# Kernel tuning notes

Measured on AMD Instinct MI355X. Metric: run time of the kernel, lower is better.

The kernel has to match this reference:

```python
import jax, jax.numpy as jnp
import numpy as np

N = 50000       # nodes
E = 1600000     # directed edges (avg degree 32)
H = 2           # heads (layers 1-2)
F_IN = 128
F_HID = 64      # per-head hidden channels
F_OUT = 64
SCALE = 0.05


def setup_inputs() -> dict:
    key = jax.random.key(0)
    ks = jax.random.split(key, 15)

    def p(k, shape):
        return jax.random.normal(k, shape, jnp.float32) * SCALE

    x = jax.random.normal(ks[0], (N, F_IN), jnp.float32)
    edge_index = jax.random.randint(ks[1], (2, E), 0, N, dtype=jnp.int64)
    return dict(
        x=x,
        W1=p(ks[2], (F_IN, H * F_HID)), as1=p(ks[3], (H, F_HID)), ad1=p(ks[4], (H, F_HID)), b1=p(ks[5], (H * F_HID,)),
        W2=p(ks[6], (H * F_HID, H * F_HID)), as2=p(ks[7], (H, F_HID)), ad2=p(ks[8], (H, F_HID)), b2=p(ks[9], (H * F_HID,)),
        W3=p(ks[10], (H * F_HID, F_OUT)), as3=p(ks[11], (1, F_OUT)), ad3=p(ks[12], (1, F_OUT)), b3=p(ks[13], (F_OUT,)),
        edge_index=edge_index,
    )


def gat_layer(x, W, a_src, a_dst, b, src, dst, heads, f_out):
    """One PyG-style GATConv (concat=True, negative_slope=0.2), dropout off (eval)."""
    n = x.shape[0]
    h = (x @ W).reshape(n, heads, f_out)                 # [N,H,F]
    al_s = jnp.einsum('nhf,hf->nh', h, a_src)            # (x_j * att_src).sum(-1)
    al_d = jnp.einsum('nhf,hf->nh', h, a_dst)
    e = jax.nn.leaky_relu(al_s[src] + al_d[dst], 0.2)    # [Etot,H]
    # segment softmax over incoming edges of each dst node
    m = jax.lax.stop_gradient(jax.ops.segment_max(e, dst, num_segments=n))
    ee = jnp.exp(e - m[dst])
    denom = jax.ops.segment_sum(ee, dst, num_segments=n)
    alpha = ee / (denom[dst] + 1e-16)                    # [Etot,H]
    out = jax.ops.segment_sum(h[src] * alpha[:, :, None], dst, num_segments=n)
    return out.reshape(n, heads * f_out) + b


def reference(x, W1, as1, ad1, b1, W2, as2, ad2, b2, W3, as3, ad3, b3, edge_index):
    # add_self_loops=True (PyG default): same augmented edge set for all layers
    loops = jnp.arange(N, dtype=edge_index.dtype)
    src = jnp.concatenate([edge_index[0], loops])
    dst = jnp.concatenate([edge_index[1], loops])
    h = jax.nn.elu(gat_layer(x, W1, as1, ad1, b1, src, dst, H, F_HID))
    h = jax.nn.elu(gat_layer(h, W2, as2, ad2, b2, src, dst, H, F_HID))
    h = jax.nn.elu(gat_layer(h, W3, as3, ad3, b3, src, dst, 1, F_OUT))
    return h
```

## Files before the change

kernel.cpp:

```cpp
#include <hip/hip_runtime.h>
#include <hip/hip_bf16.h>
#include <hip/hip_fp16.h>


#define ELU(x) ((x) > 0.f ? (x) : (__expf(x) - 1.f))
#define BSH 8
#define CHK 8192

typedef _Float16 f16x8 __attribute__((ext_vector_type(8)));
typedef float    f32x4 __attribute__((ext_vector_type(4)));
typedef float    f32x2 __attribute__((ext_vector_type(2)));

__device__ inline unsigned int f16x4_to_fp8(__half2 h0, __half2 h1) {
    float2 a = __half22float2(h0), b = __half22float2(h1);
    unsigned int r = __builtin_amdgcn_cvt_pk_fp8_f32(a.x, a.y, 0, false);
    r = __builtin_amdgcn_cvt_pk_fp8_f32(b.x, b.y, r, true);
    return r;
}

__global__ __launch_bounds__(1024) void phase0(
    const float* __restrict__ W1, __half* __restrict__ Wt1,
    const float* __restrict__ W2, __half* __restrict__ Wt2,
    const float* __restrict__ W3, __half* __restrict__ Wt3,
    const int* __restrict__ ei, int* __restrict__ bhist_rows, int E_)
{
    const int t = threadIdx.x;
    const int b = blockIdx.x;
    if (b < 40) {
        int idx = b * 1024 + t;
        const float* W; __half* Wt; int N;
        if (idx < 16384)      { W = W1; Wt = Wt1; N = 128; }
        else if (idx < 32768) { W = W2; Wt = Wt2; N = 128; idx -= 16384; }
        else                  { W = W3; Wt = Wt3; N = 64;  idx -= 32768; }
        int nn = idx >> 7, k = idx & 127;
        Wt[idx] = __float2half(W[k * N + nn]);
    } else {
        __shared__ int cnt[256];
        int hb = b - 40;
        if (t < 256) cnt[t] = 0;
        __syncthreads();
        const int e0 = hb * CHK;
        for (int i = t; i < CHK; i += 1024) {
            int e = e0 + i;
            if (e >= E_) break;
            atomicAdd(&cnt[ei[E_ + e] >> BSH], 1);
        }
        __syncthreads();
        if (t < 256) bhist_rows[hb * 256 + t] = cnt[t];
    }
}

__global__ __launch_bounds__(1024) void scan_bases(
    const int* __restrict__ bhist_rows, int* __restrict__ boff,
    int* __restrict__ bases, int* __restrict__ part, int HB, int n, int NB)
{
    __shared__ int part4[4][256];
    __shared__ int tot[256];
    __shared__ int col[256];
    const int t = threadIdx.x;
    const int b = blockIdx.x;

    {
        const int tcol = t & 255, grp = t >> 8;
        int v = 0;
        for (int r = grp; r < HB; r += 4) v += bhist_rows[r * 256 + tcol];
        part4[grp][tcol] = v;
    }
    __syncthreads();
    if (t < 256) {
        int v = part4[0][t] + part4[1][t] + part4[2][t] + part4[3][t];
        int nodes_t = n - (t << BSH);
        nodes_t = nodes_t < 0 ? 0 : (nodes_t > 256 ? 256 : nodes_t);
        tot[t] = (t < NB) ? (v + nodes_t) : 0;
    }
    __syncthreads();
    for (int d = 1; d < 256; d <<= 1) {
        int x = 0;
        if (t < 256 && t >= d) x = tot[t - d];
        __syncthreads();
        if (t < 256 && t >= d) tot[t] += x;
        __syncthreads();
    }
    if (b == 0) {
        if (t < NB) boff[t + 1] = tot[t];
        if (t == 0) boff[0] = 0;
    }
    const int base0 = (b > 0) ? tot[b - 1] : 0;
    const int bend  = tot[b];

    if (t < 256) col[t] = (t < HB) ? bhist_rows[t * 256 + b] : 0;
    __syncthreads();
    for (int d = 1; d < 256; d <<= 1) {
        int x = 0;
        if (t < 256 && t >= d) x = col[t - d];
        __syncthreads();
        if (t < 256 && t >= d) col[t] += x;
        __syncthreads();
    }
    if (t < HB) {
        int c = bhist_rows[t * 256 + b];
        bases[b * HB + t] = base0 + col[t] - c;
    }

    const int n0 = b << BSH;
    const int nodes = min(256, n - n0);
    const int sl0 = bend - nodes;
    if (t < nodes) part[sl0 + t] = (n0 + t) | (t << 16);
}

__global__ __launch_bounds__(1024) void edge_partition(
    const int* __restrict__ ei, const int* __restrict__ bases,
    int* __restrict__ part, int E_, int HB, int NB)
{
    __shared__ int cnt[256];
    __shared__ int sbase[256];
    const int t = threadIdx.x;
    const int hb = blockIdx.x;
    if (t < 256) {
        cnt[t] = 0;
        sbase[t] = (t < NB) ? bases[t * HB + hb] : 0;
    }
    __syncthreads();
    const int e0 = hb * CHK;
    for (int i = t; i < CHK; i += 1024) {
        int e = e0 + i;
        if (e >= E_) break;
        int src = ei[e], dst = ei[E_ + e];
        int b = dst >> BSH;
        int pos = sbase[b] + atomicAdd(&cnt[b], 1);
        part[pos] = src | ((dst & 255) << 16);
    }
}

__global__ __launch_bounds__(1024) void bucket_fill(
    const int* __restrict__ boff, const int* __restrict__ part,
    unsigned short* __restrict__ csr, int* __restrict__ off, int n)
{
    __shared__ int sm[256];
    __shared__ int cur[256];
    __shared__ int slice[12544];
    const int t = threadIdx.x;
    const int b = blockIdx.x;
    const int n0 = b << BSH;
    const int nodes = min(256, n - n0);
    const int off0 = boff[b];
    const int sz = boff[b + 1] - off0;

    if (t < 256) cur[t] = 0;
    __syncthreads();
    for (int i = t; i < sz; i += 1024)
        atomicAdd(&cur[(part[off0 + i] >> 16) & 255], 1);
    __syncthreads();
    int v = 0;
    if (t < 256) { v = cur[t]; sm[t] = v; }
    __syncthreads();
    for (int d = 1; d < 256; d <<= 1) {
        int x = 0;
        if (t < 256 && t >= d) x = sm[t - d];
        __syncthreads();
        if (t < 256 && t >= d) sm[t] += x;
        __syncthreads();
    }
    if (t < 256) {
        const int excl = sm[t] - v;
        if (t < nodes) off[n0 + t] = off0 + excl;
        if (t == nodes - 1) off[n0 + nodes] = off0 + sz;
        cur[t] = excl;
    }
    __syncthreads();

    if (sz <= 12544) {
        for (int i = t; i < sz; i += 1024) {
            int p  = part[off0 + i];
            int dl = (p >> 16) & 255;
            int pos = atomicAdd(&cur[dl], 1);
            slice[pos] = p & 0xFFFF;
        }
        __syncthreads();
        for (int i = t; i < sz; i += 1024)
            csr[off0 + i] = (unsigned short)slice[i];
    } else {
        for (int i = t; i < sz; i += 1024) {
            int p  = part[off0 + i];
            int dl = (p >> 16) & 255;
            int pos = atomicAdd(&cur[dl], 1);
            csr[off0 + pos] = (unsigned short)(p & 0xFFFF);
        }
    }
}

__global__ __launch_bounds__(256) void gemm1_mfma(
    const float* __restrict__ A, const __half* __restrict__ Wt,
    unsigned char* __restrict__ Hout, const float* __restrict__ a_s,
    const float* __restrict__ a_d, float* __restrict__ alS,
    float* __restrict__ alD, int nrows)
{
    constexpr int N = 128, NT = 8, WR = 136;
    __shared__ _Float16 wt[N * WR];
    __shared__ _Float16 hst[4][16 * WR];

    const int t = threadIdx.x, w = t >> 6, l = t & 63;
    const int q = l >> 4, n = l & 15;
    const int node0 = blockIdx.x * 64;
    const int row_base = node0 + w * 16;

    for (int i = t; i < N * 16; i += 256) {
        int r = i >> 4, c = i & 15;
        float4 v = *(const float4*)&Wt[r * 128 + c * 8];
        *(float4*)&wt[r * WR + c * 8] = v;
    }
    __syncthreads();

    f32x4 acc[NT];
#pragma unroll
    for (int ct = 0; ct < NT; ct++) acc[ct] = (f32x4){0.f, 0.f, 0.f, 0.f};

    int arow = row_base + n; if (arow >= nrows) arow = nrows - 1;
    const float* Ap = A + (size_t)arow * 128 + q * 8;
#pragma unroll
    for (int ks = 0; ks < 4; ks++) {
        float4 va = *(const float4*)(Ap + ks * 32);
        float4 vb = *(const float4*)(Ap + ks * 32 + 4);
        f16x8 a = { (_Float16)va.x, (_Float16)va.y, (_Float16)va.z, (_Float16)va.w,
                    (_Float16)vb.x, (_Float16)vb.y, (_Float16)vb.z, (_Float16)vb.w };
#pragma unroll
        for (int ct = 0; ct < NT; ct++) {
            f16x8 bb = *(const f16x8*)&wt[(ct * 16 + n) * WR + ks * 32 + q * 8];
            acc[ct] = __builtin_amdgcn_mfma_f32_16x16x32_f16(a, bb, acc[ct], 0, 0, 0);
        }
    }

    float asv[NT], adv[NT];
#pragma unroll
    for (int ct = 0; ct < NT; ct++) {
        asv[ct] = a_s[ct * 16 + n];
        adv[ct] = a_d[ct * 16 + n];
    }
#pragma unroll
    for (int r = 0; r < 4; r++) {
        int grow = row_base + q * 4 + r;
        float s0 = 0.f, d0 = 0.f, s1 = 0.f, d1 = 0.f;
#pragma unroll
        for (int ct = 0; ct < NT; ct++) {
            float v = acc[ct][r];
            float ps = v * asv[ct], pd = v * adv[ct];
            if (ct >= 4) { s1 += ps; d1 += pd; }
            else         { s0 += ps; d0 += pd; }
        }
#pragma unroll
        for (int m = 1; m < 16; m <<= 1) {
            s0 += __shfl_xor(s0, m); d0 += __shfl_xor(d0, m);
            s1 += __shfl_xor(s1, m); d1 += __shfl_xor(d1, m);
        }
        if (n == 0 && grow < nrows) {
            alS[grow * 2] = s0;     alD[grow * 2] = d0;
            alS[grow * 2 + 1] = s1; alD[grow * 2 + 1] = d1;
        }
    }

#pragma unroll
    for (int ct = 0; ct < NT; ct++)
#pragma unroll
        for (int r = 0; r < 4; r++)
            hst[w][(q * 4 + r) * WR + ct * 16 + n] = (_Float16)acc[ct][r];
    __syncthreads();
    {
        int row = l >> 2, c = l & 3;
        int grow = row_base + row;
        if (grow < nrows) {
#pragma unroll
            for (int i = 0; i < 4; i++) {
                float4 v = *(float4*)&hst[w][row * WR + c * 32 + i * 8];
                const __half2* hp = (const __half2*)&v;
                uint2 o;
                o.x = f16x4_to_fp8(hp[0], hp[1]);
                o.y = f16x4_to_fp8(hp[2], hp[3]);
                *(uint2*)&Hout[(size_t)grow * 128 + c * 32 + i * 8] = o;
            }
        }
    }
}

template<int OUTN>
__global__ __launch_bounds__(256) void gat_gather_gemm(
    const int* __restrict__ off, const unsigned short* __restrict__ csr,
    const unsigned char* __restrict__ h, const float* __restrict__ alS,
    const float* __restrict__ alD, const float* __restrict__ bias,
    const __half* __restrict__ Wt, const float* __restrict__ a_s,
    const float* __restrict__ a_d, unsigned char* __restrict__ Hout,
    float* __restrict__ alSo, float* __restrict__ alDo, int n)
{
    constexpr int HF = 128, WR = 136;
    constexpr int CTW = OUTN / 64;
    constexpr int CPW = OUTN / 4;
    constexpr int C = 768;
    __shared__ _Float16 actT[16 * WR];
    __shared__ float red_s[4][16], red_d[4][16];
    __shared__ int soff[17];
    __shared__ unsigned short esrc[C];
    __shared__ float ew[2][C];

    const int t = threadIdx.x;
    const int node0 = blockIdx.x * 16;

    if (t < 17) {
        int nd = node0 + t; nd = nd < n ? nd : n;
        soff[t] = off[nd];
    }
    __syncthreads();
    const int blk0 = soff[0];
    const int blkE = soff[16] - blk0;

    const int l = t & 15;
    const int nl = t >> 4;
    const int c0 = l * 8;
    const int head = l >> 3;
    const int s0 = soff[nl] - blk0;
    const int s1 = soff[nl + 1] - blk0;

    float a0 = 0.f, a1 = 0.f, a2 = 0.f, a3 = 0.f;
    float a4 = 0.f, a5 = 0.f, a6 = 0.f, a7 = 0.f, wsum = 0.f;

    for (int cbase = 0; cbase < blkE; cbase += C) {
        const int cend = min(blkE, cbase + C);

        for (int i = cbase + t; i < cend; i += 256) {
            int src = csr[blk0 + i];
            int lo = 0, hi = 16;
            while (hi - lo > 1) {
                int mid = (lo + hi) >> 1;
                if (soff[mid] - blk0 <= i) lo = mid; else hi = mid;
            }
            int dst = node0 + lo;
            float2 as2 = *(const float2*)&alS[src * 2];
            float2 ad2 = *(const float2*)&alD[dst * 2];
            float e0 = as2.x + ad2.x; e0 = e0 > 0.f ? e0 : 0.2f * e0;
            float e1 = as2.y + ad2.y; e1 = e1 > 0.f ? e1 : 0.2f * e1;
            esrc[i - cbase] = (unsigned short)src;
            ew[0][i - cbase] = __expf(e0);
            ew[1][i - cbase] = __expf(e1);
        }
        __syncthreads();

        const int lo = (s0 > cbase ? s0 : cbase) - cbase;
        const int hi = (s1 < cend ? s1 : cend) - cbase;
        if (lo < hi) {
            int sk[4]; float wk[4]; uint2 hv[4];
#pragma unroll
            for (int k = 0; k < 4; k++) {
                int jj = lo + k < hi ? lo + k : hi - 1;
                sk[k] = esrc[jj];
                wk[k] = (lo + k < hi) ? ew[head][jj] : 0.f;
            }
#pragma unroll
            for (int k = 0; k < 4; k++)
                hv[k] = *(const uint2*)&h[(size_t)sk[k] * HF + c0];

            for (int j = lo; j < hi; j += 4) {
                int ns[4]; float nw[4]; uint2 nv[4];
#pragma unroll
                for (int k = 0; k < 4; k++) {
                    int jj = j + 4 + k < hi ? j + 4 + k : hi - 1;
                    ns[k] = esrc[jj];
                    nw[k] = (j + 4 + k < hi) ? ew[head][jj] : 0.f;
                }
#pragma unroll
                for (int k = 0; k < 4; k++)
                    nv[k] = *(const uint2*)&h[(size_t)ns[k] * HF + c0];
#pragma unroll
                for (int k = 0; k < 4; k++) {
                    float w = wk[k];
                    f32x2 f0 = __builtin_amdgcn_cvt_pk_f32_fp8(hv[k].x, false);
                    f32x2 f1 = __builtin_amdgcn_cvt_pk_f32_fp8(hv[k].x, true);
                    f32x2 f2 = __builtin_amdgcn_cvt_pk_f32_fp8(hv[k].y, false);
                    f32x2 f3 = __builtin_amdgcn_cvt_pk_f32_fp8(hv[k].y, true);
                    a0 = fmaf(w, f0.x, a0); a1 = fmaf(w, f0.y, a1);
                    a2 = fmaf(w, f1.x, a2); a3 = fmaf(w, f1.y, a3);
                    a4 = fmaf(w, f2.x, a4); a5 = fmaf(w, f2.y, a5);
                    a6 = fmaf(w, f3.x, a6); a7 = fmaf(w, f3.y, a7);
                    wsum += w;
                }
#pragma unroll
                for (int k = 0; k < 4; k++) { sk[k] = ns[k]; wk[k] = nw[k]; hv[k] = nv[k]; }
            }
        }
        __syncthreads();
    }

    {
        const float inv = 1.f / (wsum + 1e-16f);
        float4 b0 = *(const float4*)&bias[c0];
        float4 b1 = *(const float4*)&bias[c0 + 4];
        float o[8];
        o[0] = ELU(fmaf(a0, inv, b0.x));
        o[1] = ELU(fmaf(a1, inv, b0.y));
        o[2] = ELU(fmaf(a2, inv, b0.z));
        o[3] = ELU(fmaf(a3, inv, b0.w));
        o[4] = ELU(fmaf(a4, inv, b1.x));
        o[5] = ELU(fmaf(a5, inv, b1.y));
        o[6] = ELU(fmaf(a6, inv, b1.z));
        o[7] = ELU(fmaf(a7, inv, b1.w));
        __half2 p[4];
#pragma unroll
        for (int k = 0; k < 4; k++) p[k] = __floats2half2_rn(o[2 * k], o[2 * k + 1]);
        *(float4*)&actT[nl * WR + l * 8] = *(float4*)p;
    }
    __syncthreads();

    const int w = t >> 6, l64 = t & 63, q = l64 >> 4, nn = l64 & 15;
    const __half* Wp = Wt + (size_t)(w * CPW + nn) * 128 + q * 8;
    f32x4 acc[CTW];
#pragma unroll
    for (int ct = 0; ct < CTW; ct++) acc[ct] = (f32x4){0.f, 0.f, 0.f, 0.f};
#pragma unroll
    for (int ks = 0; ks < 4; ks++) {
        f16x8 a = *(const f16x8*)&actT[nn * WR + ks * 32 + q * 8];
#pragma unroll
        for (int ct = 0; ct < CTW; ct++) {
            f16x8 bb = *(const f16x8*)(Wp + ct * 16 * 128 + ks * 32);
            acc[ct] = __builtin_amdgcn_mfma_f32_16x16x32_f16(a, bb, acc[ct], 0, 0, 0);
        }
    }

    float asv[CTW], adv2[CTW];
#pragma unroll
    for (int ct = 0; ct < CTW; ct++) {
        asv[ct]  = a_s[w * CPW + ct * 16 + nn];
        adv2[ct] = a_d[w * CPW + ct * 16 + nn];
    }
#pragma unroll
    for (int r = 0; r < 4; r++) {
        float s = 0.f, d = 0.f;
#pragma unroll
        for (int ct = 0; ct < CTW; ct++) {
            float vv = acc[ct][r];
            s = fmaf(vv, asv[ct], s);
            d = fmaf(vv, adv2[ct], d);
        }
#pragma unroll
        for (int m = 1; m < 16; m <<= 1) {
            s += __shfl_xor(s, m);
            d += __shfl_xor(d, m);
        }
        if (nn == 0) { red_s[w][q * 4 + r] = s; red_d[w][q * 4 + r] = d; }
    }
    __syncthreads();

#pragma unroll
    for (int ct = 0; ct < CTW; ct++)
#pragma unroll
        for (int r = 0; r < 4; r++)
            actT[(q * 4 + r) * WR + w * CPW + ct * 16 + nn] = (_Float16)acc[ct][r];
    if (OUTN == 128) {
        if (t < 32) {
            int m = t & 15, hh = t >> 4;
            int grow = node0 + m;
            if (grow < n) {
                alSo[grow * 2 + hh] = red_s[2 * hh][m] + red_s[2 * hh + 1][m];
                alDo[grow * 2 + hh] = red_d[2 * hh][m] + red_d[2 * hh + 1][m];
            }
        }
    } else {
        if (t < 16) {
            int grow = node0 + t;
            if (grow < n) {
                alSo[grow] = red_s[0][t] + red_s[1][t] + red_s[2][t] + red_s[3][t];
                alDo[grow] = red_d[0][t] + red_d[1][t] + red_d[2][t] + red_d[3][t];
            }
        }
    }
    __syncthreads();

    if (OUTN == 128) {
        int row = t >> 4, c = t & 15;
        int grow = node0 + row;
        if (grow < n) {
            float4 v8 = *(float4*)&actT[row * WR + c * 8];
            const __half2* hp = (const __half2*)&v8;
            uint2 o;
            o.x = f16x4_to_fp8(hp[0], hp[1]);
            o.y = f16x4_to_fp8(hp[2], hp[3]);
            *(uint2*)&Hout[(size_t)grow * 128 + c * 8] = o;
        }
    } else {
        if (t < 128) {
            int row = t >> 3, c = t & 7;
            int grow = node0 + row;
            if (grow < n) {
                float4 v8 = *(float4*)&actT[row * WR + c * 8];
                const __half2* hp = (const __half2*)&v8;
                uint2 o;
                o.x = f16x4_to_fp8(hp[0], hp[1]);
                o.y = f16x4_to_fp8(hp[2], hp[3]);
                *(uint2*)&Hout[(size_t)grow * 64 + c * 8] = o;
            }
        }
    }
}

__global__ __launch_bounds__(256) void gat_gather_out(
    const int* __restrict__ off, const unsigned short* __restrict__ csr,
    const unsigned char* __restrict__ h, const float* __restrict__ alS,
    const float* __restrict__ alD, const float* __restrict__ b,
    float* __restrict__ out, int n)
{
    constexpr int HF = 64;
    constexpr int C = 1280;
    __shared__ int soff[33];
    __shared__ unsigned short esrc[C];
    __shared__ float ew[C];

    const int t = threadIdx.x;
    const int node0 = blockIdx.x * 32;

    if (t < 33) {
        int nd = node0 + t; nd = nd < n ? nd : n;
        soff[t] = off[nd];
    }
    __syncthreads();
    const int blk0 = soff[0];
    const int blkE = soff[32] - blk0;

    const int l = t & 7;
    const int nl = t >> 3;
    const int node = node0 + nl;
    const int c0 = l * 8;
    const int s0 = soff[nl] - blk0;
    const int s1 = soff[nl + 1] - blk0;

    float a0 = 0.f, a1 = 0.f, a2 = 0.f, a3 = 0.f;
    float a4 = 0.f, a5 = 0.f, a6 = 0.f, a7 = 0.f, wsum = 0.f;

    for (int cbase = 0; cbase < blkE; cbase += C) {
        const int cend = min(blkE, cbase + C);

        for (int i = cbase + t; i < cend; i += 256) {
            int src = csr[blk0 + i];
            int lo = 0, hi = 32;
            while (hi - lo > 1) {
                int mid = (lo + hi) >> 1;
                if (soff[mid] - blk0 <= i) lo = mid; else hi = mid;
            }
            int dst = node0 + lo;
            float e = alS[src] + alD[dst];
            e = e > 0.f ? e : 0.2f * e;
            esrc[i - cbase] = (unsigned short)src;
            ew[i - cbase] = __expf(e);
        }
        __syncthreads();

        const int lo = (s0 > cbase ? s0 : cbase) - cbase;
        const int hi = (s1 < cend ? s1 : cend) - cbase;
        if (lo < hi) {
            int sk[4]; float wk[4]; uint2 hv[4];
#pragma unroll
            for (int k = 0; k < 4; k++) {
                int jj = lo + k < hi ? lo + k : hi - 1;
                sk[k] = esrc[jj];
                wk[k] = (lo + k < hi) ? ew[jj] : 0.f;
            }
#pragma unroll
            for (int k = 0; k < 4; k++)
                hv[k] = *(const uint2*)&h[(size_t)sk[k] * HF + c0];

            for (int j = lo; j < hi; j += 4) {
                int ns[4]; float nw[4]; uint2 nv[4];
#pragma unroll
                for (int k = 0; k < 4; k++) {
                    int jj = j + 4 + k < hi ? j + 4 + k : hi - 1;
                    ns[k] = esrc[jj];
                    nw[k] = (j + 4 + k < hi) ? ew[jj] : 0.f;
                }
#pragma unroll
                for (int k = 0; k < 4; k++)
                    nv[k] = *(const uint2*)&h[(size_t)ns[k] * HF + c0];
#pragma unroll
                for (int k = 0; k < 4; k++) {
                    float w = wk[k];
                    f32x2 f0 = __builtin_amdgcn_cvt_pk_f32_fp8(hv[k].x, false);
                    f32x2 f1 = __builtin_amdgcn_cvt_pk_f32_fp8(hv[k].x, true);
                    f32x2 f2 = __builtin_amdgcn_cvt_pk_f32_fp8(hv[k].y, false);
                    f32x2 f3 = __builtin_amdgcn_cvt_pk_f32_fp8(hv[k].y, true);
                    a0 = fmaf(w, f0.x, a0); a1 = fmaf(w, f0.y, a1);
                    a2 = fmaf(w, f1.x, a2); a3 = fmaf(w, f1.y, a3);
                    a4 = fmaf(w, f2.x, a4); a5 = fmaf(w, f2.y, a5);
                    a6 = fmaf(w, f3.x, a6); a7 = fmaf(w, f3.y, a7);
                    wsum += w;
                }
#pragma unroll
                for (int k = 0; k < 4; k++) { sk[k] = ns[k]; wk[k] = nw[k]; hv[k] = nv[k]; }
            }
        }
        __syncthreads();
    }

    if (node >= n) return;
    const float inv = 1.f / (wsum + 1e-16f);
    float4 b0 = *(const float4*)&b[c0];
    float4 b1 = *(const float4*)&b[c0 + 4];
    float4 o0, o1;
    o0.x = ELU(fmaf(a0, inv, b0.x));
    o0.y = ELU(fmaf(a1, inv, b0.y));
    o0.z = ELU(fmaf(a2, inv, b0.z));
    o0.w = ELU(fmaf(a3, inv, b0.w));
    o1.x = ELU(fmaf(a4, inv, b1.x));
    o1.y = ELU(fmaf(a5, inv, b1.y));
    o1.z = ELU(fmaf(a6, inv, b1.z));
    o1.w = ELU(fmaf(a7, inv, b1.w));
    *(float4*)&out[(size_t)node * HF + c0]     = o0;
    *(float4*)&out[(size_t)node * HF + c0 + 4] = o1;
}

extern "C" void kernel_launch(void* const* d_in, const int* in_sizes, int n_in,
                              void* d_out, int out_size, void* d_ws, size_t ws_size,
                              hipStream_t stream)
{
    const float* x   = (const float*)d_in[0];
    const float* W1  = (const float*)d_in[1];
    const float* as1 = (const float*)d_in[2];
    const float* ad1 = (const float*)d_in[3];
    const float* b1  = (const float*)d_in[4];
    const float* W2  = (const float*)d_in[5];
    const float* as2 = (const float*)d_in[6];
    const float* ad2 = (const float*)d_in[7];
    const float* b2  = (const float*)d_in[8];
    const float* W3  = (const float*)d_in[9];
    const float* as3 = (const float*)d_in[10];
    const float* ad3 = (const float*)d_in[11];
    const float* b3  = (const float*)d_in[12];
    const int*   ei  = (const int*)d_in[13];
    float* out = (float*)d_out;

    const int N_   = in_sizes[0] / 128;
    const int E_   = in_sizes[13] / 2;
    const int Etot = E_ + N_;
    const int NB   = (N_ + 255) >> BSH;
    const int HB   = (E_ + CHK - 1) / CHK;

    char* ws = (char*)d_ws;
    size_t o = 0;
    auto alloc = [&](size_t bytes) { void* p = ws + o; o += (bytes + 255) & ~255ull; return p; };
    unsigned char* h1 = (unsigned char*)alloc((size_t)N_ * 128);
    unsigned char* h2 = (unsigned char*)alloc((size_t)N_ * 128);
    unsigned char* h3 = (unsigned char*)alloc((size_t)N_ * 64);
    __half* Wt1   = (__half*)alloc((size_t)128 * 128 * 2);
    __half* Wt2   = (__half*)alloc((size_t)128 * 128 * 2);
    __half* Wt3   = (__half*)alloc((size_t)64 * 128 * 2);
    float* alSa   = (float*)alloc((size_t)N_ * 2 * 4);
    float* alDa   = (float*)alloc((size_t)N_ * 2 * 4);
    float* alSb   = (float*)alloc((size_t)N_ * 2 * 4);
    float* alDb   = (float*)alloc((size_t)N_ * 2 * 4);
    int*   offb   = (int*)alloc((size_t)(N_ + 1) * 4);
    int*   bhrows = (int*)alloc((size_t)HB * 256 * 4);
    int*   boff   = (int*)alloc((size_t)257 * 4);
    int*   bases  = (int*)alloc((size_t)256 * HB * 4);
    int*   part   = (int*)alloc((size_t)Etot * 4);
    unsigned short* csr = (unsigned short*)alloc((size_t)Etot * 2);

    const dim3 blk(256);
    const dim3 blk1k(1024);

    phase0<<<40 + HB, blk1k, 0, stream>>>(W1, Wt1, W2, Wt2, W3, Wt3, ei, bhrows, E_);
    scan_bases<<<NB, blk1k, 0, stream>>>(bhrows, boff, bases, part, HB, N_, NB);
    edge_partition<<<HB, blk1k, 0, stream>>>(ei, bases, part, E_, HB, NB);
    bucket_fill<<<NB, blk1k, 0, stream>>>(boff, part, csr, offb, N_);

    gemm1_mfma<<<(N_ + 63) / 64, blk, 0, stream>>>(x, Wt1, h1, as1, ad1, alSa, alDa, N_);
    gat_gather_gemm<128><<<(N_ + 15) / 16, blk, 0, stream>>>(
        offb, csr, h1, alSa, alDa, b1, Wt2, as2, ad2, h2, alSb, alDb, N_);
    gat_gather_gemm<64><<<(N_ + 15) / 16, blk, 0, stream>>>(
        offb, csr, h2, alSb, alDb, b2, Wt3, as3, ad3, h3, alSa, alDa, N_);
    gat_gather_out<<<(N_ + 31) / 32, blk, 0, stream>>>(
        offb, csr, h3, alSa, alDa, b3, out, N_);
}
```

Before: 251.2 us.

## Merge edge partition and first-layer GEMM into one heterogeneous launch

The edge-partition kernel and the layer-1 MFMA GEMM are merged into a single launch. The first HB blocks do the edge partitioning and the remaining blocks compute the GEMM and attention logits, with shared memory unioned between the two roles. This removes one kernel launch and lets the independent GEMM work overlap with the partitioning on idle CUs. In exchange, GEMM blocks now run at 1024 threads with only 256 active, which wastes thread slots and may reduce occupancy.

```diff
diff --git a/kernel.cpp b/kernel.cpp
--- a/kernel.cpp
+++ b/kernel.cpp
@@ -108,27 +108,125 @@
     if (t < nodes) part[sl0 + t] = (n0 + t) | (t << 16);
 }
 
-__global__ __launch_bounds__(1024) void edge_partition(
+__global__ __launch_bounds__(1024) void partition_gemm1(
     const int* __restrict__ ei, const int* __restrict__ bases,
-    int* __restrict__ part, int E_, int HB, int NB)
+    int* __restrict__ part, int E_, int HB, int NB,
+    const float* __restrict__ A, const __half* __restrict__ Wt,
+    unsigned char* __restrict__ Hout, const float* __restrict__ a_s,
+    const float* __restrict__ a_d, float* __restrict__ alS,
+    float* __restrict__ alD, int nrows)
 {
-    __shared__ int cnt[256];
-    __shared__ int sbase[256];
+    constexpr int N = 128, NT = 8, WR = 136;
+    __shared__ union SM {
+        struct { int cnt[256]; int sbase[256]; } p;
+        struct { _Float16 wt[N * WR]; _Float16 hst[4][16 * WR]; } g;
+    } sm;
     const int t = threadIdx.x;
-    const int hb = blockIdx.x;
+
+    if ((int)blockIdx.x < HB) {
+        const int hb = blockIdx.x;
+        if (t < 256) {
+            sm.p.cnt[t] = 0;
+            sm.p.sbase[t] = (t < NB) ? bases[t * HB + hb] : 0;
+        }
+        __syncthreads();
+        const int e0 = hb * CHK;
+        for (int i = t; i < CHK; i += 1024) {
+            int e = e0 + i;
+            if (e >= E_) break;
+            int src = ei[e], dst = ei[E_ + e];
+            int b = dst >> BSH;
+            int pos = sm.p.sbase[b] + atomicAdd(&sm.p.cnt[b], 1);
+            part[pos] = src | ((dst & 255) << 16);
+        }
+        return;
+    }
+
+    _Float16* wt = sm.g.wt;
+    const int node0 = (blockIdx.x - HB) * 64;
+
+    for (int i = t; i < N * 16; i += 1024) {
+        int r = i >> 4, c = i & 15;
+        float4 v = *(const float4*)&Wt[r * 128 + c * 8];
+        *(float4*)&wt[r * WR + c * 8] = v;
+    }
+    __syncthreads();
+
     if (t < 256) {
-        cnt[t] = 0;
-        sbase[t] = (t < NB) ? bases[t * HB + hb] : 0;
-    }
-    __syncthreads();
-    const int e0 = hb * CHK;
-    for (int i = t; i < CHK; i += 1024) {
-        int e = e0 + i;
-        if (e >= E_) break;
-        int src = ei[e], dst = ei[E_ + e];
-        int b = dst >> BSH;
-        int pos = sbase[b] + atomicAdd(&cnt[b], 1);
-        part[pos] = src | ((dst & 255) << 16);
+        const int w = t >> 6, l = t & 63;
+        const int q = l >> 4, n = l & 15;
+        const int row_base = node0 + w * 16;
+
+        f32x4 acc[NT];
+#pragma unroll
+        for (int ct = 0; ct < NT; ct++) acc[ct] = (f32x4){0.f, 0.f, 0.f, 0.f};
+
+        int arow = row_base + n; if (arow >= nrows) arow = nrows - 1;
+        const float* Ap = A + (size_t)arow * 128 + q * 8;
+#pragma unroll
+        for (int ks = 0; ks < 4; ks++) {
+            float4 va = *(const float4*)(Ap + ks * 32);
+            float4 vb = *(const float4*)(Ap + ks * 32 + 4);
+            f16x8 a = { (_Float16)va.x, (_Float16)va.y, (_Float16)va.z, (_Float16)va.w,
+                        (_Float16)vb.x, (_Float16)vb.y, (_Float16)vb.z, (_Float16)vb.w };
+#pragma unroll
+            for (int ct = 0; ct < NT; ct++) {
+                f16x8 bb = *(const f16x8*)&wt[(ct * 16 + n) * WR + ks * 32 + q * 8];
+                acc[ct] = __builtin_amdgcn_mfma_f32_16x16x32_f16(a, bb, acc[ct], 0, 0, 0);
+            }
+        }
+
+        float asv[NT], adv[NT];
+#pragma unroll
+        for (int ct = 0; ct < NT; ct++) {
+            asv[ct] = a_s[ct * 16 + n];
+            adv[ct] = a_d[ct * 16 + n];
+        }
+#pragma unroll
+        for (int r = 0; r < 4; r++) {
+            int grow = row_base + q * 4 + r;
+            float s0 = 0.f, d0 = 0.f, s1 = 0.f, d1 = 0.f;
+#pragma unroll
+            for (int ct = 0; ct < NT; ct++) {
+                float v = acc[ct][r];
+                float ps = v * asv[ct], pd = v * adv[ct];
+                if (ct >= 4) { s1 += ps; d1 += pd; }
+                else         { s0 += ps; d0 += pd; }
+            }
+#pragma unroll
+            for (int m = 1; m < 16; m <<= 1) {
+                s0 += __shfl_xor(s0, m); d0 += __shfl_xor(d0, m);
+                s1 += __shfl_xor(s1, m); d1 += __shfl_xor(d1, m);
+            }
+            if (n == 0 && grow < nrows) {
+                alS[grow * 2] = s0;     alD[grow * 2] = d0;
+                alS[grow * 2 + 1] = s1; alD[grow * 2 + 1] = d1;
+            }
+        }
+
+#pragma unroll
+        for (int ct = 0; ct < NT; ct++)
+#pragma unroll
+            for (int r = 0; r < 4; r++)
+                sm.g.hst[w][(q * 4 + r) * WR + ct * 16 + n] = (_Float16)acc[ct][r];
+    }
+    __syncthreads();
+    if (t < 256) {
+        const int w = t >> 6, l = t & 63;
+        const int row_base = node0 + w * 16;
+        int row = l >> 2, c = l & 3;
+        int grow = row_base + row;
+        if (grow < nrows) {
+#pragma unroll
+            for (int i = 0; i < 4; i++) {
+                float4 v = *(float4*)&sm.g.hst[w][row * WR + c * 32 + i * 8];
+                const __half2* hp = (const __half2*)&v;
+                uint2 o;
+                o.x = f16x4_to_fp8(hp[0], hp[1]);
+                o.y = f16x4_to_fp8(hp[2], hp[3]);
+                *(uint2*)&Hout[(size_t)grow * 128 + c * 32 + i * 8] = o;
+            }
+        }
     }
 }
 
@@ -185,98 +283,6 @@
             int dl = (p >> 16) & 255;
             int pos = atomicAdd(&cur[dl], 1);
             csr[off0 + pos] = (unsigned short)(p & 0xFFFF);
-        }
-    }
-}
-
-__global__ __launch_bounds__(256) void gemm1_mfma(
-    const float* __restrict__ A, const __half* __restrict__ Wt,
-    unsigned char* __restrict__ Hout, const float* __restrict__ a_s,
-    const float* __restrict__ a_d, float* __restrict__ alS,
-    float* __restrict__ alD, int nrows)
-{
-    constexpr int N = 128, NT = 8, WR = 136;
-    __shared__ _Float16 wt[N * WR];
-    __shared__ _Float16 hst[4][16 * WR];
-
-    const int t = threadIdx.x, w = t >> 6, l = t & 63;
-    const int q = l >> 4, n = l & 15;
-    const int node0 = blockIdx.x * 64;
-    const int row_base = node0 + w * 16;
-
-    for (int i = t; i < N * 16; i += 256) {
-        int r = i >> 4, c = i & 15;
-        float4 v = *(const float4*)&Wt[r * 128 + c * 8];
-        *(float4*)&wt[r * WR + c * 8] = v;
-    }
-    __syncthreads();
-
-    f32x4 acc[NT];
-#pragma unroll
-    for (int ct = 0; ct < NT; ct++) acc[ct] = (f32x4){0.f, 0.f, 0.f, 0.f};
-
-    int arow = row_base + n; if (arow >= nrows) arow = nrows - 1;
-    const float* Ap = A + (size_t)arow * 128 + q * 8;
-#pragma unroll
-    for (int ks = 0; ks < 4; ks++) {
-        float4 va = *(const float4*)(Ap + ks * 32);
-        float4 vb = *(const float4*)(Ap + ks * 32 + 4);
-        f16x8 a = { (_Float16)va.x, (_Float16)va.y, (_Float16)va.z, (_Float16)va.w,
-                    (_Float16)vb.x, (_Float16)vb.y, (_Float16)vb.z, (_Float16)vb.w };
-#pragma unroll
-        for (int ct = 0; ct < NT; ct++) {
-            f16x8 bb = *(const f16x8*)&wt[(ct * 16 + n) * WR + ks * 32 + q * 8];
-            acc[ct] = __builtin_amdgcn_mfma_f32_16x16x32_f16(a, bb, acc[ct], 0, 0, 0);
-        }
-    }
-
-    float asv[NT], adv[NT];
-#pragma unroll
-    for (int ct = 0; ct < NT; ct++) {
-        asv[ct] = a_s[ct * 16 + n];
-        adv[ct] = a_d[ct * 16 + n];
-    }
-#pragma unroll
-    for (int r = 0; r < 4; r++) {
-        int grow = row_base + q * 4 + r;
-        float s0 = 0.f, d0 = 0.f, s1 = 0.f, d1 = 0.f;
-#pragma unroll
-        for (int ct = 0; ct < NT; ct++) {
-            float v = acc[ct][r];
-            float ps = v * asv[ct], pd = v * adv[ct];
-            if (ct >= 4) { s1 += ps; d1 += pd; }
-            else         { s0 += ps; d0 += pd; }
-        }
-#pragma unroll
-        for (int m = 1; m < 16; m <<= 1) {
-            s0 += __shfl_xor(s0, m); d0 += __shfl_xor(d0, m);
-            s1 += __shfl_xor(s1, m); d1 += __shfl_xor(d1, m);
-        }
-        if (n == 0 && grow < nrows) {
-            alS[grow * 2] = s0;     alD[grow * 2] = d0;
-            alS[grow * 2 + 1] = s1; alD[grow * 2 + 1] = d1;
-        }
-    }
-
-#pragma unroll
-    for (int ct = 0; ct < NT; ct++)
-#pragma unroll
-        for (int r = 0; r < 4; r++)
-            hst[w][(q * 4 + r) * WR + ct * 16 + n] = (_Float16)acc[ct][r];
-    __syncthreads();
-    {
-        int row = l >> 2, c = l & 3;
-        int grow = row_base + row;
-        if (grow < nrows) {
-#pragma unroll
-            for (int i = 0; i < 4; i++) {
-                float4 v = *(float4*)&hst[w][row * WR + c * 32 + i * 8];
-                const __half2* hp = (const __half2*)&v;
-                uint2 o;
-                o.x = f16x4_to_fp8(hp[0], hp[1]);
-                o.y = f16x4_to_fp8(hp[2], hp[3]);
-                *(uint2*)&Hout[(size_t)grow * 128 + c * 32 + i * 8] = o;
-            }
         }
     }
 }
@@ -659,13 +665,15 @@
 
     const dim3 blk(256);
     const dim3 blk1k(1024);
+    const int G1 = (N_ + 63) / 64;
 
     phase0<<<40 + HB, blk1k, 0, stream>>>(W1, Wt1, W2, Wt2, W3, Wt3, ei, bhrows, E_);
     scan_bases<<<NB, blk1k, 0, stream>>>(bhrows, boff, bases, part, HB, N_, NB);
-    edge_partition<<<HB, blk1k, 0, stream>>>(ei, bases, part, E_, HB, NB);
+    partition_gemm1<<<HB + G1, blk1k, 0, stream>>>(
+        ei, bases, part, E_, HB, NB,
+        x, Wt1, h1, as1, ad1, alSa, alDa, N_);
     bucket_fill<<<NB, blk1k, 0, stream>>>(boff, part, csr, offb, N_);
 
-    gemm1_mfma<<<(N_ + 63) / 64, blk, 0, stream>>>(x, Wt1, h1, as1, ad1, alSa, alDa, N_);
     gat_gather_gemm<128><<<(N_ + 15) / 16, blk, 0, stream>>>(
         offb, csr, h1, alSa, alDa, b1, Wt2, as2, ad2, h2, alSb, alDb, N_);
     gat_gather_gemm<64><<<(N_ + 15) / 16, blk, 0, stream>>>(
```

Result: no change. 253.1 us (+0.8%).
